# Performance work log

Hardware: AMD Instinct MI355X
Metric: run time of the kernel (lower is better)

Reference implementation:

```python
import jax, jax.numpy as jnp
import numpy as np

N_HARMONIC = 8
FRAME_SHIFT = 240
SR = 24000
ALPHA = 0.1
SIGMA = 0.003
B = 32
N_FRAMES = 500


def setup_inputs() -> dict:
    key = jax.random.key(0)
    k1, k2, k3, k4 = jax.random.split(key, 4)
    u = jax.random.uniform(k1, (B, N_FRAMES), dtype=jnp.float32)
    f0s = jnp.where(u < 0.1, 0.0, 80.0 + u * 320.0)
    # random phase per harmonic in [-pi, 0], phi[0] = 0 (matches torch init)
    phi = jax.random.uniform(k2, (N_HARMONIC,), dtype=jnp.float32) * (-np.pi)
    phi = phi.at[0].set(0.0)
    amplitude = jax.random.normal(k3, (N_HARMONIC + 1,), dtype=jnp.float32)
    # per-harmonic gaussian noise N(0, sigma) at sample rate
    noise = SIGMA * jax.random.normal(
        k4, (N_HARMONIC, B, N_FRAMES * FRAME_SHIFT), dtype=jnp.float32)
    return {"f0s": f0s, "phi": phi, "amplitude": amplitude, "noise": noise}


def reference(f0s, phi, amplitude, noise):
    # upsample frame-rate f0 to sample rate: [B, n_frames] -> [B, T]
    f0_up = jnp.repeat(f0s, FRAME_SHIFT, axis=1)
    # cumsum is linear in harmonic index: compute once, scale by (i+1)
    cs = jnp.cumsum(2.0 * np.pi * f0_up / SR, axis=1)            # [B, T]
    k = jnp.arange(1, N_HARMONIC + 1, dtype=f0s.dtype)           # [H]
    sin_all = jnp.sin(k[:, None, None] * cs[None] + phi[:, None, None])  # [H, B, T]
    pos = (f0_up > 0).astype(f0s.dtype)                          # [B, T]
    zero = (f0_up == 0).astype(f0s.dtype)                        # [B, T]
    # excitation per harmonic: voiced -> alpha*sin + noise; unvoiced -> scaled noise
    exc = (ALPHA * sin_all + noise) * pos + zero * (ALPHA / (3.0 * SIGMA)) * noise
    out = jnp.tanh(jnp.einsum('h,hbt->bt', amplitude[:N_HARMONIC], exc)
                   + amplitude[N_HARMONIC])
    return out
```

## Files before the change

### kernel.cpp

```cpp
#include <hip/hip_runtime.h>
#include <math.h>

constexpr int   BB    = 32;
constexpr int   NF    = 500;
constexpr int   FS    = 240;
constexpr int   TT    = NF * FS;
constexpr int   HH    = 8;
constexpr float ALPHA = 0.1f;

constexpr int SPT = 8;
constexpr int BLK = 256;

__device__ __forceinline__ float sin_rev(float fr) {
#if __has_builtin(__builtin_amdgcn_sinf)
    return __builtin_amdgcn_sinf(fr);
#else
    return __sinf(fr * 6.28318530717958647692f);
#endif
}

__device__ __forceinline__ float tanh_fast(float x) {
    const float e = __expf(2.0f * x);
#if __has_builtin(__builtin_amdgcn_rcpf)
    const float r = __builtin_amdgcn_rcpf(e + 1.0f);
#else
    const float r = 1.0f / (e + 1.0f);
#endif
    return fmaf(-2.0f, r, 1.0f);
}

__global__ __launch_bounds__(BLK) void synth_fused(const float* __restrict__ f0s,
                                                   const float* __restrict__ phi,
                                                   const float* __restrict__ amp,
                                                   const float* __restrict__ noise,
                                                   float* __restrict__ out) {
    const int b    = blockIdx.y;
    const int tid  = threadIdx.x;
    const int lane = tid & 63;
    const int wv   = tid >> 6;

    __shared__ float2 sfr[NF];
    __shared__ double wtot[BLK / 64];

    {
        const float  TWO_PI_F = 6.28318530717958647692f;
        const double INV_2PI  = 0.15915494309189533576;

        const int fi = 2 * tid;
        double d0 = 0.0, d1 = 0.0;
        if (fi < NF) {
            const float dphi = (TWO_PI_F * f0s[b * NF + fi]) / 24000.0f;
            d0 = (double)dphi * INV_2PI;
        }
        if (fi + 1 < NF) {
            const float dphi = (TWO_PI_F * f0s[b * NF + fi + 1]) / 24000.0f;
            d1 = (double)dphi * INV_2PI;
        }

        const double s = (d0 + d1) * 240.0;
        double run = s;
        for (int delta = 1; delta < 64; delta <<= 1) {
            const double o = __shfl_up(run, delta, 64);
            if (lane >= delta) run += o;
        }
        if (lane == 63) wtot[wv] = run;
        __syncthreads();

        double woff = 0.0;
        for (int w2 = 0; w2 < wv; ++w2) woff += wtot[w2];
        double pref = woff + (run - s);

        if (fi < NF) {
            const double fx0 = pref - rint(pref);
            sfr[fi] = make_float2((float)fx0, (float)d0);
            if (fi + 1 < NF) {
                const double p1  = pref + d0 * 240.0;
                const double fx1 = p1 - rint(p1);
                sfr[fi + 1] = make_float2((float)fx1, (float)d1);
            }
        }
        __syncthreads();
    }

    const int t = (blockIdx.x * BLK + tid) * SPT;
    if (t >= TT) return;

    const int f = t / FS;
    const int j = t - f * FS;
    const size_t base = (size_t)b * TT + t;

    const float2 fd = sfr[f];
    const float  dr = fd.y;
    const bool   voiced = (dr > 0.0f);

    float cs[SPT];
    cs[0] = fd.x + (float)(j + 1) * dr;
#pragma unroll
    for (int e = 1; e < SPT; ++e) cs[e] = cs[e - 1] + dr;

    const float INV2PIf = 0.15915494309189533576f;

    float sdot[SPT], ndot[SPT];
#pragma unroll
    for (int e = 0; e < SPT; ++e) { sdot[e] = 0.f; ndot[e] = 0.f; }

#pragma unroll
    for (int h = 0; h < HH; ++h) {
        const float a  = amp[h];
        const float ph = phi[h] * INV2PIf;
        const float kf = (float)(h + 1);

        const float4* p = reinterpret_cast<const float4*>(
            noise + (size_t)h * (BB * (size_t)TT) + base);
        const float4 m0 = p[0];
        const float4 m1 = p[1];

        ndot[0] = fmaf(a, m0.x, ndot[0]);
        ndot[1] = fmaf(a, m0.y, ndot[1]);
        ndot[2] = fmaf(a, m0.z, ndot[2]);
        ndot[3] = fmaf(a, m0.w, ndot[3]);
        ndot[4] = fmaf(a, m1.x, ndot[4]);
        ndot[5] = fmaf(a, m1.y, ndot[5]);
        ndot[6] = fmaf(a, m1.z, ndot[6]);
        ndot[7] = fmaf(a, m1.w, ndot[7]);

#pragma unroll
        for (int e = 0; e < SPT; ++e) {
            const float r  = fmaf(kf, cs[e], ph);
            const float fx = r - rintf(r);
            sdot[e] = fmaf(a, sin_rev(fx), sdot[e]);
        }
    }

    const float a8 = amp[HH];
    const float UV = (float)(0.1 / (3.0 * 0.003));

    float tmp[SPT];
#pragma unroll
    for (int e = 0; e < SPT; ++e) {
        const float x = voiced ? fmaf(ALPHA, sdot[e], ndot[e]) : UV * ndot[e];
        tmp[e] = tanh_fast(x + a8);
    }

    float4* ov = reinterpret_cast<float4*>(out + base);
    ov[0] = make_float4(tmp[0], tmp[1], tmp[2], tmp[3]);
    ov[1] = make_float4(tmp[4], tmp[5], tmp[6], tmp[7]);
}

extern "C" void kernel_launch(void* const* d_in, const int* in_sizes, int n_in,
                              void* d_out, int out_size, void* d_ws, size_t ws_size,
                              hipStream_t stream) {
    const float* f0s   = (const float*)d_in[0];
    const float* phi   = (const float*)d_in[1];
    const float* amp   = (const float*)d_in[2];
    const float* noise = (const float*)d_in[3];
    float* out = (float*)d_out;

    const int blocks_x = (TT / SPT + BLK - 1) / BLK;
    dim3 grid(blocks_x, BB);
    synth_fused<<<grid, BLK, 0, stream>>>(f0s, phi, amp, noise, out);
}
```

Baseline: 28.23 us.

## Use persistent per-row chunks with double-buffered noise loads and rotated harmonic order

```diff
diff --git a/kernel.cpp b/kernel.cpp
--- a/kernel.cpp
+++ b/kernel.cpp
@@ -8,8 +8,11 @@
 constexpr int   HH    = 8;
 constexpr float ALPHA = 0.1f;
 
-constexpr int SPT = 8;
-constexpr int BLK = 256;
+constexpr int BLK     = 256;
+constexpr int CPR     = 24;
+constexpr int CH_SAMP = TT / CPR;
+constexpr int CH_QUAD = CH_SAMP / 4;
+constexpr int NIT     = (CH_QUAD + BLK - 1) / BLK;
 
 __device__ __forceinline__ float sin_rev(float fr) {
 #if __has_builtin(__builtin_amdgcn_sinf)
@@ -34,18 +37,21 @@
                                                    const float* __restrict__ amp,
                                                    const float* __restrict__ noise,
                                                    float* __restrict__ out) {
-    const int b    = blockIdx.y;
+    const int bid  = blockIdx.x;
     const int tid  = threadIdx.x;
     const int lane = tid & 63;
     const int wv   = tid >> 6;
 
+    const int b = bid / CPR;
+    const int c = bid % CPR;
+
     __shared__ float2 sfr[NF];
     __shared__ double wtot[BLK / 64];
 
+    const float  TWO_PI_F = 6.28318530717958647692f;
+    const double INV_2PI  = 0.15915494309189533576;
+
     {
-        const float  TWO_PI_F = 6.28318530717958647692f;
-        const double INV_2PI  = 0.15915494309189533576;
-
         const int fi = 2 * tid;
         double d0 = 0.0, d1 = 0.0;
         if (fi < NF) {
@@ -82,69 +88,89 @@
         __syncthreads();
     }
 
-    const int t = (blockIdx.x * BLK + tid) * SPT;
-    if (t >= TT) return;
+    const float INV2PIf = 0.15915494309189533576f;
+    const int   rot     = (bid * 4 + wv) & 7;
+    const size_t HSTR   = (size_t)BB * (size_t)TT;
 
-    const int f = t / FS;
-    const int j = t - f * FS;
-    const size_t base = (size_t)b * TT + t;
-
-    const float2 fd = sfr[f];
-    const float  dr = fd.y;
-    const bool   voiced = (dr > 0.0f);
-
-    float cs[SPT];
-    cs[0] = fd.x + (float)(j + 1) * dr;
+    float a_r[HH], ph_r[HH], kf_r[HH];
 #pragma unroll
-    for (int e = 1; e < SPT; ++e) cs[e] = cs[e - 1] + dr;
-
-    const float INV2PIf = 0.15915494309189533576f;
-
-    float sdot[SPT], ndot[SPT];
-#pragma unroll
-    for (int e = 0; e < SPT; ++e) { sdot[e] = 0.f; ndot[e] = 0.f; }
-
-#pragma unroll
-    for (int h = 0; h < HH; ++h) {
-        const float a  = amp[h];
-        const float ph = phi[h] * INV2PIf;
-        const float kf = (float)(h + 1);
-
-        const float4* p = reinterpret_cast<const float4*>(
-            noise + (size_t)h * (BB * (size_t)TT) + base);
-        const float4 m0 = p[0];
-        const float4 m1 = p[1];
-
-        ndot[0] = fmaf(a, m0.x, ndot[0]);
-        ndot[1] = fmaf(a, m0.y, ndot[1]);
-        ndot[2] = fmaf(a, m0.z, ndot[2]);
-        ndot[3] = fmaf(a, m0.w, ndot[3]);
-        ndot[4] = fmaf(a, m1.x, ndot[4]);
-        ndot[5] = fmaf(a, m1.y, ndot[5]);
-        ndot[6] = fmaf(a, m1.z, ndot[6]);
-        ndot[7] = fmaf(a, m1.w, ndot[7]);
-
-#pragma unroll
-        for (int e = 0; e < SPT; ++e) {
-            const float r  = fmaf(kf, cs[e], ph);
-            const float fx = r - rintf(r);
-            sdot[e] = fmaf(a, sin_rev(fx), sdot[e]);
-        }
+    for (int hh = 0; hh < HH; ++hh) {
+        const int h = (hh + rot) & 7;
+        a_r[hh]  = amp[h];
+        ph_r[hh] = phi[h] * INV2PIf;
+        kf_r[hh] = (float)(h + 1);
     }
-
     const float a8 = amp[HH];
     const float UV = (float)(0.1 / (3.0 * 0.003));
 
-    float tmp[SPT];
-#pragma unroll
-    for (int e = 0; e < SPT; ++e) {
-        const float x = voiced ? fmaf(ALPHA, sdot[e], ndot[e]) : UV * ndot[e];
-        tmp[e] = tanh_fast(x + a8);
+    const size_t rowbase = (size_t)b * TT + (size_t)c * CH_SAMP;
+
+#define LOAD_M(M, IT)                                                          \
+    {                                                                          \
+        const int q = min((IT) * BLK + tid, CH_QUAD - 1);                      \
+        const size_t off = rowbase + (size_t)q * 4;                            \
+        _Pragma("unroll")                                                      \
+        for (int hh = 0; hh < HH; ++hh) {                                      \
+            const int h = (hh + rot) & 7;                                      \
+            M[hh] = *reinterpret_cast<const float4*>(noise + (size_t)h * HSTR + off); \
+        }                                                                      \
     }
 
-    float4* ov = reinterpret_cast<float4*>(out + base);
-    ov[0] = make_float4(tmp[0], tmp[1], tmp[2], tmp[3]);
-    ov[1] = make_float4(tmp[4], tmp[5], tmp[6], tmp[7]);
+#define BODY_M(M, IT)                                                          \
+    {                                                                          \
+        const int  qr  = (IT) * BLK + tid;                                     \
+        const bool act = (qr < CH_QUAD);                                       \
+        const int  q   = act ? qr : (CH_QUAD - 1);                             \
+        const int  t_loc = q * 4;                                              \
+        const int  t  = c * CH_SAMP + t_loc;                                   \
+        const int  f  = t / FS;                                                \
+        const int  j  = t - f * FS;                                            \
+        const float2 fd = sfr[f];                                              \
+        const float  dr = fd.y;                                                \
+        const bool   voiced = (dr > 0.0f);                                     \
+        float cs[4];                                                           \
+        cs[0] = fd.x + (float)(j + 1) * dr;                                    \
+        cs[1] = cs[0] + dr;  cs[2] = cs[1] + dr;  cs[3] = cs[2] + dr;          \
+        float sdot[4] = {0.f, 0.f, 0.f, 0.f};                                  \
+        float ndot[4] = {0.f, 0.f, 0.f, 0.f};                                  \
+        _Pragma("unroll")                                                      \
+        for (int hh = 0; hh < HH; ++hh) {                                      \
+            const float a  = a_r[hh];                                          \
+            const float ph = ph_r[hh];                                         \
+            const float kf = kf_r[hh];                                         \
+            ndot[0] = fmaf(a, M[hh].x, ndot[0]);                               \
+            ndot[1] = fmaf(a, M[hh].y, ndot[1]);                               \
+            ndot[2] = fmaf(a, M[hh].z, ndot[2]);                               \
+            ndot[3] = fmaf(a, M[hh].w, ndot[3]);                               \
+            _Pragma("unroll")                                                  \
+            for (int e = 0; e < 4; ++e) {                                      \
+                const float r  = fmaf(kf, cs[e], ph);                          \
+                const float fx = r - rintf(r);                                 \
+                sdot[e] = fmaf(a, sin_rev(fx), sdot[e]);                       \
+            }                                                                  \
+        }                                                                      \
+        float tmp[4];                                                          \
+        _Pragma("unroll")                                                      \
+        for (int e = 0; e < 4; ++e) {                                          \
+            const float x = voiced ? fmaf(ALPHA, sdot[e], ndot[e]) : UV * ndot[e]; \
+            tmp[e] = tanh_fast(x + a8);                                        \
+        }                                                                      \
+        if (act) {                                                             \
+            *reinterpret_cast<float4*>(out + (size_t)b * TT + t) =             \
+                make_float4(tmp[0], tmp[1], tmp[2], tmp[3]);                   \
+        }                                                                      \
+    }
+
+    float4 mA[HH], mB[HH];
+    LOAD_M(mA, 0)
+    LOAD_M(mB, 1)  BODY_M(mA, 0)
+    LOAD_M(mA, 2)  BODY_M(mB, 1)
+    LOAD_M(mB, 3)  BODY_M(mA, 2)
+    LOAD_M(mA, 4)  BODY_M(mB, 3)
+    BODY_M(mA, 4)
+
+#undef LOAD_M
+#undef BODY_M
 }
 
 extern "C" void kernel_launch(void* const* d_in, const int* in_sizes, int n_in,
@@ -156,7 +182,6 @@
     const float* noise = (const float*)d_in[3];
     float* out = (float*)d_out;
 
-    const int blocks_x = (TT / SPT + BLK - 1) / BLK;
-    dim3 grid(blocks_x, BB);
-    synth_fused<<<grid, BLK, 0, stream>>>(f0s, phi, amp, noise, out);
+    const int nblocks = BB * CPR;
+    synth_fused<<<nblocks, BLK, 0, stream>>>(f0s, phi, amp, noise, out);
 }
```

New measurement: 27.61 us. 2.2% less time.
